# Optimization experiments

Hardware: AMD Instinct MI355X
Metric: run time of the kernel (lower is better)

## Reference

```python
import jax, jax.numpy as jnp
import numpy as np

N_WIRES = 4
DIM = 2 ** N_WIRES  # 16
# ZSIGN[w, b] = +1/-1 eigenvalue of Pauli-Z on wire w for basis state b (qubit 0 = MSB)
_bits = np.array([[(b >> (N_WIRES - 1 - w)) & 1 for b in range(DIM)] for w in range(N_WIRES)])
ZSIGN = jnp.asarray(1.0 - 2.0 * _bits, dtype=jnp.float32)  # [4, 16]
CNOT4 = jnp.asarray(np.array([[1, 0, 0, 0], [0, 1, 0, 0], [0, 0, 0, 1], [0, 0, 1, 0]], dtype=np.float32))


def _apply_1q(state, U2, w):
    # state [..., 16]; apply 2x2 gate U2 on wire w
    batch = state.shape[:-1]
    s = state.reshape(batch + (2,) * N_WIRES)
    s = jnp.moveaxis(s, w - N_WIRES, -1)
    s = s @ U2.astype(s.dtype).T
    s = jnp.moveaxis(s, -1, w - N_WIRES)
    return s.reshape(batch + (DIM,))


def _apply_2q(state, U4, c, t):
    # state [..., 16]; apply 4x4 gate U4 on wires (c=control-axis-first, t)
    batch = state.shape[:-1]
    s = state.reshape(batch + (2,) * N_WIRES)
    s = jnp.moveaxis(s, (c - N_WIRES, t - N_WIRES), (-2, -1))
    sh = s.shape
    s = s.reshape(sh[:-2] + (4,))
    s = s @ U4.astype(s.dtype).T
    s = s.reshape(sh)
    s = jnp.moveaxis(s, (-2, -1), (c - N_WIRES, t - N_WIRES))
    return s.reshape(batch + (DIM,))


def _product_state(qs):
    # kron of per-qubit 2-vectors -> [..., 16]
    s = qs[0]
    for q in qs[1:]:
        o = s[..., :, None] * q[..., None, :]
        s = o.reshape(o.shape[:-2] + (o.shape[-2] * o.shape[-1],))
    return s


def _measure_z(state):
    if jnp.iscomplexobj(state):
        probs = state.real ** 2 + state.imag ** 2
    else:
        probs = state ** 2
    return probs.astype(jnp.float32) @ ZSIGN.T  # [..., 4]


def _quanv(x, rl_params):
    # x [B, 784]; 2x2 stride-2 patches of 28x28 image, RY encode, fixed 8-op
    # 'random layer' (RY(rl_params[w]) on wire w then CNOT(w, w+1 mod 4)), measure Z.
    B = x.shape[0]
    img = x.reshape(B, 14, 2, 14, 2)
    patches = img.transpose(0, 1, 3, 2, 4).reshape(B, 196, 4)  # [(r,c),(r,c+1),(r+1,c),(r+1,c+1)]
    half = patches * 0.5
    q = jnp.stack([jnp.cos(half), jnp.sin(half)], axis=-1)  # RY(theta)|0> is real, [B,196,4,2]
    st = _product_state([q[..., w, :] for w in range(N_WIRES)])  # [B,196,16] float32
    for w in range(N_WIRES):
        th = rl_params[w] * 0.5
        ct, sn = jnp.cos(th), jnp.sin(th)
        U2 = jnp.stack([jnp.stack([ct, -sn]), jnp.stack([sn, ct])])
        st = _apply_1q(st, U2, w)
        st = _apply_2q(st, CNOT4, w, (w + 1) % N_WIRES)
    return _measure_z(st)  # [B, 196, 4]


def _qlayer(ang, theta):
    # RX(ang_w) encode + trainable RX(theta_w) fuse into RX(ang+theta); CNOT ring; <Z>
    half = (ang + theta) * 0.5  # [B, 4]
    c = jnp.cos(half).astype(jnp.complex64)
    s = (-1j) * jnp.sin(half).astype(jnp.complex64)
    q = jnp.stack([c, s], axis=-1)  # [B, 4, 2]
    st = _product_state([q[:, w, :] for w in range(N_WIRES)])  # [B, 16] complex64
    for w in range(N_WIRES):
        st = _apply_2q(st, CNOT4, w, (w + 1) % N_WIRES)
    return _measure_z(st)  # [B, 4]


def _forward(x, rl_params, lin_W, lin_b, qtheta):
    B = x.shape[0]
    qfeat = _quanv(x, rl_params)  # [B, 196, 4]
    xs = jnp.transpose(qfeat, (1, 0, 2))  # [196, B, 4] sequence for quantum LSTM
    h0 = jnp.zeros((B, 4), jnp.float32)
    c0 = jnp.zeros((B, 4), jnp.float32)

    def step(carry, xt):
        hx, cx = carry
        comb = jnp.concatenate([xt, hx], axis=1)  # [B, 8]
        f = jax.nn.sigmoid(_qlayer(comb @ lin_W[0] + lin_b[0], qtheta[0]))
        i = jax.nn.sigmoid(_qlayer(comb @ lin_W[1] + lin_b[1], qtheta[1]))
        g = jnp.tanh(_qlayer(comb @ lin_W[2] + lin_b[2], qtheta[2]))
        o = jax.nn.sigmoid(_qlayer(comb @ lin_W[3] + lin_b[3], qtheta[3]))
        cx = f * cx + i * g
        hx = o * jnp.tanh(cx)
        return (hx, cx), hx

    (hx, cx), _ = jax.lax.scan(step, (h0, c0), xs)
    # torch.tensor([float(v) ...]) detaches -> stop_gradient; mean over batch
    w = jax.lax.stop_gradient(jnp.mean(hx, axis=0))  # [4]
    # EstimatorQNN: ry(inp_i) then rx(w_i) per qubit, observable ZZZZ -> prod cos(inp)cos(w)
    inp = x[:, :N_WIRES]
    return jnp.prod(jnp.cos(inp) * jnp.cos(w), axis=1, keepdims=True)  # [B, 1]


def setup_inputs() -> dict:
    key = jax.random.key(0)
    k0, k1, k2, k3 = jax.random.split(key, 4)
    B = 8192
    x = jax.random.uniform(k0, (B, 784), dtype=jnp.float32) * np.float32(np.pi)
    rl_params = jax.random.normal(k1, (4,), dtype=jnp.float32)
    lin_W = jax.random.normal(k2, (4, 8, 4), dtype=jnp.float32) * np.float32(1.0 / np.sqrt(8.0))
    lin_b = jnp.zeros((4, 4), dtype=jnp.float32)
    qtheta = jax.random.normal(k3, (4, 4), dtype=jnp.float32)
    return {"x": x, "rl_params": rl_params, "lin_W": lin_W, "lin_b": lin_b, "qtheta": qtheta}


def reference(x, rl_params, lin_W, lin_b, qtheta):
    return _forward(x, rl_params, lin_W, lin_b, qtheta)
```

## Files before the change

kernel.cpp:

```cpp
#include <hip/hip_runtime.h>
#include <math.h>

#define NPATCH 196
#define QROWS  204

typedef unsigned short ushort_t;

__device__ __forceinline__ float fast_rcp(float x) { return __builtin_amdgcn_rcpf(x); }

__device__ __forceinline__ ushort_t f2bf(float f) {
    unsigned u = __float_as_uint(f);
    u += 0x7FFFu + ((u >> 16) & 1u);
    return (ushort_t)(u >> 16);
}
__device__ __forceinline__ float bflo(unsigned v) { return __uint_as_float(v << 16); }
__device__ __forceinline__ float bfhi(unsigned v) { return __uint_as_float(v & 0xFFFF0000u); }

template<int CTRL>
__device__ __forceinline__ int dpp_i(int x) {
    return __builtin_amdgcn_update_dpp(x, x, CTRL, 0xF, 0xF, true);
}
template<int CTRL>
__device__ __forceinline__ float dpp_f(float x) {
    return __int_as_float(dpp_i<CTRL>(__float_as_int(x)));
}
#define QP_BCAST0 0x00
#define QP_BCAST1 0x55
#define QP_BCAST2 0xAA
#define QP_BCAST3 0xFF
#define ROR4      0x124
#define ROR8      0x128
#define ROR12     0x12C

#define SPB  16
#define ROWP 788

__global__ __launch_bounds__(256) void quanv_kernel(const float* __restrict__ x,
                                                    const float* __restrict__ rl,
                                                    ushort_t* __restrict__ qfeat, int B)
{
    __shared__ float tile[SPB][ROWP];
    const int tid = threadIdx.x;
    const int b0  = blockIdx.x * SPB;

#pragma unroll 4
    for (int r = 0; r < SPB; ++r) {
        if (tid < 196) {
            ((float4*)&tile[r][0])[tid] =
                ((const float4*)(x + (size_t)(b0 + r) * 784))[tid];
        }
    }
    __syncthreads();

    float rs[4], rc[4];
#pragma unroll
    for (int w = 0; w < 4; ++w) __sincosf(rl[w] * 0.5f, &rs[w], &rc[w]);

    const int s  = tid & 15;
    const int tg = tid >> 4;
    const float* row = &tile[s][0];

    for (int t = tg; t < NPATCH; t += 16) {
        int i = t / 14, j = t - i * 14;
        int o = i * 56 + j * 2;
        float a[4] = { row[o], row[o + 1], row[o + 28], row[o + 29] };

        float cw[4], sw[4];
#pragma unroll
        for (int w = 0; w < 4; ++w) __sincosf(a[w] * 0.5f, &sw[w], &cw[w]);

        float amp[16];
#pragma unroll
        for (int idx = 0; idx < 16; ++idx) {
            float v = ((idx & 8) ? sw[0] : cw[0]) * ((idx & 4) ? sw[1] : cw[1]);
            v *= ((idx & 2) ? sw[2] : cw[2]);
            v *= ((idx & 1) ? sw[3] : cw[3]);
            amp[idx] = v;
        }

#pragma unroll
        for (int w = 0; w < 4; ++w) {
            const int mask = 8 >> w;
#pragma unroll
            for (int idx = 0; idx < 16; ++idx) {
                if (!(idx & mask)) {
                    float a0 = amp[idx], a1 = amp[idx | mask];
                    amp[idx]        = rc[w] * a0 - rs[w] * a1;
                    amp[idx | mask] = rs[w] * a0 + rc[w] * a1;
                }
            }
            const int tmask = 8 >> ((w + 1) & 3);
#pragma unroll
            for (int idx = 0; idx < 16; ++idx) {
                if ((idx & mask) && !(idx & tmask)) {
                    float tmp = amp[idx];
                    amp[idx] = amp[idx | tmask];
                    amp[idx | tmask] = tmp;
                }
            }
        }

        float p[16];
#pragma unroll
        for (int idx = 0; idx < 16; ++idx) p[idx] = amp[idx] * amp[idx];
        float z0 = 0.f, z1 = 0.f, z2 = 0.f, z3 = 0.f;
#pragma unroll
        for (int idx = 0; idx < 16; ++idx) {
            z0 += (idx & 8) ? -p[idx] : p[idx];
            z1 += (idx & 4) ? -p[idx] : p[idx];
            z2 += (idx & 2) ? -p[idx] : p[idx];
            z3 += (idx & 1) ? -p[idx] : p[idx];
        }

        ushort4 outv;
        outv.x = f2bf(z0); outv.y = f2bf(z1); outv.z = f2bf(z2); outv.w = f2bf(z3);
        *(ushort4*)(qfeat + ((size_t)t * B + (b0 + s)) * 4) = outv;
    }
}

__global__ __launch_bounds__(256) void lstm_kernel(const ushort_t* __restrict__ qfeat,
                                                   const float* __restrict__ lin_W,
                                                   const float* __restrict__ lin_b,
                                                   const float* __restrict__ qtheta,
                                                   float* __restrict__ sums, int B)
{
    const int tid = threadIdx.x;
    const int gid = blockIdx.x * 256 + tid;
    const int pr  = gid >> 4;
    const int u   = (tid >> 2) & 3;
    const int k   = tid & 3;
    const int Bh  = B >> 1;

    const int j1 = dpp_i<ROR4>(u);
    const int j2 = dpp_i<ROR8>(u);
    const int j3 = dpp_i<ROR12>(u);

    const float Wx0 = lin_W[(k * 8 + 0) * 4 + u];
    const float Wx1 = lin_W[(k * 8 + 1) * 4 + u];
    const float Wx2 = lin_W[(k * 8 + 2) * 4 + u];
    const float Wx3 = lin_W[(k * 8 + 3) * 4 + u];
    const float Wh0 = lin_W[(k * 8 + 4 + u)  * 4 + u];
    const float Wh1 = lin_W[(k * 8 + 4 + j1) * 4 + u];
    const float Wh2 = lin_W[(k * 8 + 4 + j2) * 4 + u];
    const float Wh3 = lin_W[(k * 8 + 4 + j3) * 4 + u];
    const float bt  = lin_b[k * 4 + u] + qtheta[k * 4 + u];

    auto in_set = [](int j, int uu) {
        return (uu == 0) ? (j != 0) : (uu == 1) ? (j <= 1) : (uu == 2) ? (j <= 2) : true;
    };
    const bool inc0 = in_set(u,  u);
    const bool inc1 = in_set(j1, u);
    const bool inc2 = in_set(j2, u);
    const bool inc3 = in_set(j3, u);

    const float mlt = (k == 2) ?  2.0f : -1.0f;
    const float ga  = (k == 2) ? -2.0f :  1.0f;
    const float gb  = (k == 2) ?  1.0f :  0.0f;

    const uint4* qp = (const uint4*)qfeat;
    uint4 r0 = qp[(size_t)0 * Bh + pr];
    uint4 r1 = qp[(size_t)1 * Bh + pr];
    uint4 r2 = qp[(size_t)2 * Bh + pr];
    uint4 r3 = qp[(size_t)3 * Bh + pr];
    uint4 r4 = qp[(size_t)4 * Bh + pr];
    uint4 r5 = qp[(size_t)5 * Bh + pr];
    uint4 r6 = qp[(size_t)6 * Bh + pr];

    float cxa = 0.f, hxa = 0.f;
    float cxb = 0.f, hxb = 0.f;

    auto step = [&](uint4& buf, int tn) {
        float ax0 = bflo(buf.x), ax1 = bfhi(buf.x), ax2 = bflo(buf.y), ax3 = bfhi(buf.y);
        float bx0 = bflo(buf.z), bx1 = bfhi(buf.z), bx2 = bflo(buf.w), bx3 = bfhi(buf.w);
        buf = qp[(size_t)tn * Bh + pr];

        float ha1 = dpp_f<ROR4>(hxa), hb1 = dpp_f<ROR4>(hxb);
        float ha2 = dpp_f<ROR8>(hxa), hb2 = dpp_f<ROR8>(hxb);
        float ha3 = dpp_f<ROR12>(hxa), hb3 = dpp_f<ROR12>(hxb);

        float as0 = fmaf(ax0, Wx0, bt);
        float bs0 = fmaf(bx0, Wx0, bt);
        float as1 = ax1 * Wx1;
        float bs1 = bx1 * Wx1;
        as0 = fmaf(ax2, Wx2, as0);  bs0 = fmaf(bx2, Wx2, bs0);
        as1 = fmaf(ax3, Wx3, as1);  bs1 = fmaf(bx3, Wx3, bs1);
        as0 = fmaf(hxa, Wh0, as0);  bs0 = fmaf(hxb, Wh0, bs0);
        as1 = fmaf(ha1, Wh1, as1);  bs1 = fmaf(hb1, Wh1, bs1);
        as0 = fmaf(ha2, Wh2, as0);  bs0 = fmaf(hb2, Wh2, bs0);
        as1 = fmaf(ha3, Wh3, as1);  bs1 = fmaf(hb3, Wh3, bs1);
        float cva = __cosf(as0 + as1);
        float cvb = __cosf(bs0 + bs1);

        float ca1 = dpp_f<ROR4>(cva),  cb1 = dpp_f<ROR4>(cvb);
        float ca2 = dpp_f<ROR8>(cva),  cb2 = dpp_f<ROR8>(cvb);
        float ca3 = dpp_f<ROR12>(cva), cb3 = dpp_f<ROR12>(cvb);
        float za = (inc0 ? cva : 1.0f) * (inc1 ? ca1 : 1.0f)
                 * ((inc2 ? ca2 : 1.0f) * (inc3 ? ca3 : 1.0f));
        float zb = (inc0 ? cvb : 1.0f) * (inc1 ? cb1 : 1.0f)
                 * ((inc2 ? cb2 : 1.0f) * (inc3 ? cb3 : 1.0f));

        float ea  = __expf(za * mlt);
        float eb  = __expf(zb * mlt);
        float gva = fmaf(fast_rcp(1.0f + ea), ga, gb);
        float gvb = fmaf(fast_rcp(1.0f + eb), ga, gb);

        float fa = dpp_f<QP_BCAST0>(gva), fb = dpp_f<QP_BCAST0>(gvb);
        float ia = dpp_f<QP_BCAST1>(gva), ib = dpp_f<QP_BCAST1>(gvb);
        float g_a = dpp_f<QP_BCAST2>(gva), g_b = dpp_f<QP_BCAST2>(gvb);
        float oa = dpp_f<QP_BCAST3>(gva), ob = dpp_f<QP_BCAST3>(gvb);

        cxa = fmaf(fa, cxa, ia * g_a);
        cxb = fmaf(fb, cxb, ib * g_b);
        float ta = fmaf(-2.0f, fast_rcp(1.0f + __expf(2.0f * cxa)), 1.0f);
        float tb = fmaf(-2.0f, fast_rcp(1.0f + __expf(2.0f * cxb)), 1.0f);
        hxa = oa * ta;
        hxb = ob * tb;
    };

    for (int t = 0; t < NPATCH; t += 7) {
        step(r0, t + 7);
        step(r1, t + 8);
        step(r2, t + 9);
        step(r3, t + 10);
        step(r4, t + 11);
        step(r5, t + 12);
        step(r6, t + 13);
    }

    float v = hxa + hxb;
    v += __shfl_xor(v, 16, 64);
    v += __shfl_xor(v, 32, 64);
    if ((tid & 63) < 16 && k == 0) atomicAdd(sums + u, v);
}

__global__ __launch_bounds__(256) void final_kernel(const float* __restrict__ x,
                                                    const float* __restrict__ sums,
                                                    float* __restrict__ out,
                                                    int B, float invB)
{
    int b = blockIdx.x * blockDim.x + threadIdx.x;
    if (b >= B) return;
    float P = cosf(sums[0] * invB) * cosf(sums[1] * invB) *
              cosf(sums[2] * invB) * cosf(sums[3] * invB);
    const float4 xi = *(const float4*)(x + (size_t)b * 784);
    out[b] = P * cosf(xi.x) * cosf(xi.y) * cosf(xi.z) * cosf(xi.w);
}

extern "C" void kernel_launch(void* const* d_in, const int* in_sizes, int n_in,
                              void* d_out, int out_size, void* d_ws, size_t ws_size,
                              hipStream_t stream)
{
    const float* x      = (const float*)d_in[0];
    const float* rl     = (const float*)d_in[1];
    const float* lin_W  = (const float*)d_in[2];
    const float* lin_b  = (const float*)d_in[3];
    const float* qtheta = (const float*)d_in[4];
    float* out = (float*)d_out;
    int B = in_sizes[0] / 784;

    float*    sums  = (float*)d_ws;
    ushort_t* qfeat = (ushort_t*)((char*)d_ws + 256);

    hipMemsetAsync(sums, 0, 4 * sizeof(float), stream);

    quanv_kernel<<<B / SPB, 256, 0, stream>>>(x, rl, qfeat, B);

    lstm_kernel<<<(B * 8) / 256, 256, 0, stream>>>(qfeat, lin_W, lin_b, qtheta, sums, B);

    final_kernel<<<(B + 255) / 256, 256, 0, stream>>>(x, sums, out, B, 1.0f / (float)B);
}
```

Baseline: 146.7 us.

## Fuse quanvolution and LSTM kernels through shared-memory feature staging

Merges the quanvolution kernel and the LSTM kernel into one kernel. Each block computes bf16 patch features for 32 samples into shared memory and then runs the recurrent scan from LDS rather than from a global intermediate buffer. This removes the global write and read of the feature tensor and one kernel launch. In exchange the block now reads x directly from global memory with strided float2 loads, and occupancy drops to 256 blocks of 256 threads with a large LDS footprint. The serial LSTM phase can no longer overlap with feature computation of other blocks on the same CU.

```diff
diff --git a/kernel.cpp b/kernel.cpp
--- a/kernel.cpp
+++ b/kernel.cpp
@@ -2,7 +2,7 @@
 #include <math.h>
 
 #define NPATCH 196
-#define QROWS  204
+#define TPAD   202
 
 typedef unsigned short ushort_t;
 
@@ -32,104 +32,95 @@
 #define ROR8      0x128
 #define ROR12     0x12C
 
-#define SPB  16
-#define ROWP 788
-
-__global__ __launch_bounds__(256) void quanv_kernel(const float* __restrict__ x,
-                                                    const float* __restrict__ rl,
-                                                    ushort_t* __restrict__ qfeat, int B)
+__global__ __launch_bounds__(256, 1) void fused_kernel(
+        const float* __restrict__ x,
+        const float* __restrict__ rl,
+        const float* __restrict__ lin_W,
+        const float* __restrict__ lin_b,
+        const float* __restrict__ qtheta,
+        float* __restrict__ sums, int B)
 {
-    __shared__ float tile[SPB][ROWP];
+    __shared__ alignas(16) ushort_t feat[16][TPAD][8];
+
     const int tid = threadIdx.x;
-    const int b0  = blockIdx.x * SPB;
-
-#pragma unroll 4
-    for (int r = 0; r < SPB; ++r) {
-        if (tid < 196) {
-            ((float4*)&tile[r][0])[tid] =
-                ((const float4*)(x + (size_t)(b0 + r) * 784))[tid];
+
+    {
+        const int sb    = tid >> 3;
+        const int tsub  = tid & 7;
+        const int smp   = blockIdx.x * 32 + sb;
+        const int pairb = sb >> 1;
+        const int par   = sb & 1;
+
+        float rs[4], rc[4];
+#pragma unroll
+        for (int w = 0; w < 4; ++w) __sincosf(rl[w] * 0.5f, &rs[w], &rc[w]);
+
+        const float* row = x + (size_t)smp * 784;
+
+        for (int jt = 0; jt < 25; ++jt) {
+            int t = tsub + (jt << 3);
+            if (t < NPATCH) {
+                int i = t / 14, j = t - i * 14;
+                int o = i * 56 + j * 2;
+                float2 p01 = *(const float2*)(row + o);
+                float2 p23 = *(const float2*)(row + o + 28);
+                float a[4] = { p01.x, p01.y, p23.x, p23.y };
+
+                float cw[4], sw[4];
+#pragma unroll
+                for (int w = 0; w < 4; ++w) __sincosf(a[w] * 0.5f, &sw[w], &cw[w]);
+
+                float amp[16];
+#pragma unroll
+                for (int idx = 0; idx < 16; ++idx) {
+                    float v = ((idx & 8) ? sw[0] : cw[0]) * ((idx & 4) ? sw[1] : cw[1]);
+                    v *= ((idx & 2) ? sw[2] : cw[2]);
+                    v *= ((idx & 1) ? sw[3] : cw[3]);
+                    amp[idx] = v;
+                }
+#pragma unroll
+                for (int w = 0; w < 4; ++w) {
+                    const int mask = 8 >> w;
+#pragma unroll
+                    for (int idx = 0; idx < 16; ++idx) {
+                        if (!(idx & mask)) {
+                            float a0 = amp[idx], a1 = amp[idx | mask];
+                            amp[idx]        = rc[w] * a0 - rs[w] * a1;
+                            amp[idx | mask] = rs[w] * a0 + rc[w] * a1;
+                        }
+                    }
+                    const int tmask = 8 >> ((w + 1) & 3);
+#pragma unroll
+                    for (int idx = 0; idx < 16; ++idx) {
+                        if ((idx & mask) && !(idx & tmask)) {
+                            float tmp = amp[idx];
+                            amp[idx] = amp[idx | tmask];
+                            amp[idx | tmask] = tmp;
+                        }
+                    }
+                }
+                float p[16];
+#pragma unroll
+                for (int idx = 0; idx < 16; ++idx) p[idx] = amp[idx] * amp[idx];
+                float z0 = 0.f, z1 = 0.f, z2 = 0.f, z3 = 0.f;
+#pragma unroll
+                for (int idx = 0; idx < 16; ++idx) {
+                    z0 += (idx & 8) ? -p[idx] : p[idx];
+                    z1 += (idx & 4) ? -p[idx] : p[idx];
+                    z2 += (idx & 2) ? -p[idx] : p[idx];
+                    z3 += (idx & 1) ? -p[idx] : p[idx];
+                }
+                ushort4 ov;
+                ov.x = f2bf(z0); ov.y = f2bf(z1); ov.z = f2bf(z2); ov.w = f2bf(z3);
+                *(ushort4*)&feat[pairb][t][par * 4] = ov;
+            }
         }
     }
     __syncthreads();
 
-    float rs[4], rc[4];
-#pragma unroll
-    for (int w = 0; w < 4; ++w) __sincosf(rl[w] * 0.5f, &rs[w], &rc[w]);
-
-    const int s  = tid & 15;
-    const int tg = tid >> 4;
-    const float* row = &tile[s][0];
-
-    for (int t = tg; t < NPATCH; t += 16) {
-        int i = t / 14, j = t - i * 14;
-        int o = i * 56 + j * 2;
-        float a[4] = { row[o], row[o + 1], row[o + 28], row[o + 29] };
-
-        float cw[4], sw[4];
-#pragma unroll
-        for (int w = 0; w < 4; ++w) __sincosf(a[w] * 0.5f, &sw[w], &cw[w]);
-
-        float amp[16];
-#pragma unroll
-        for (int idx = 0; idx < 16; ++idx) {
-            float v = ((idx & 8) ? sw[0] : cw[0]) * ((idx & 4) ? sw[1] : cw[1]);
-            v *= ((idx & 2) ? sw[2] : cw[2]);
-            v *= ((idx & 1) ? sw[3] : cw[3]);
-            amp[idx] = v;
-        }
-
-#pragma unroll
-        for (int w = 0; w < 4; ++w) {
-            const int mask = 8 >> w;
-#pragma unroll
-            for (int idx = 0; idx < 16; ++idx) {
-                if (!(idx & mask)) {
-                    float a0 = amp[idx], a1 = amp[idx | mask];
-                    amp[idx]        = rc[w] * a0 - rs[w] * a1;
-                    amp[idx | mask] = rs[w] * a0 + rc[w] * a1;
-                }
-            }
-            const int tmask = 8 >> ((w + 1) & 3);
-#pragma unroll
-            for (int idx = 0; idx < 16; ++idx) {
-                if ((idx & mask) && !(idx & tmask)) {
-                    float tmp = amp[idx];
-                    amp[idx] = amp[idx | tmask];
-                    amp[idx | tmask] = tmp;
-                }
-            }
-        }
-
-        float p[16];
-#pragma unroll
-        for (int idx = 0; idx < 16; ++idx) p[idx] = amp[idx] * amp[idx];
-        float z0 = 0.f, z1 = 0.f, z2 = 0.f, z3 = 0.f;
-#pragma unroll
-        for (int idx = 0; idx < 16; ++idx) {
-            z0 += (idx & 8) ? -p[idx] : p[idx];
-            z1 += (idx & 4) ? -p[idx] : p[idx];
-            z2 += (idx & 2) ? -p[idx] : p[idx];
-            z3 += (idx & 1) ? -p[idx] : p[idx];
-        }
-
-        ushort4 outv;
-        outv.x = f2bf(z0); outv.y = f2bf(z1); outv.z = f2bf(z2); outv.w = f2bf(z3);
-        *(ushort4*)(qfeat + ((size_t)t * B + (b0 + s)) * 4) = outv;
-    }
-}
-
-__global__ __launch_bounds__(256) void lstm_kernel(const ushort_t* __restrict__ qfeat,
-                                                   const float* __restrict__ lin_W,
-                                                   const float* __restrict__ lin_b,
-                                                   const float* __restrict__ qtheta,
-                                                   float* __restrict__ sums, int B)
-{
-    const int tid = threadIdx.x;
-    const int gid = blockIdx.x * 256 + tid;
-    const int pr  = gid >> 4;
-    const int u   = (tid >> 2) & 3;
-    const int k   = tid & 3;
-    const int Bh  = B >> 1;
+    const int pr = tid >> 4;
+    const int u  = (tid >> 2) & 3;
+    const int k  = tid & 3;
 
     const int j1 = dpp_i<ROR4>(u);
     const int j2 = dpp_i<ROR8>(u);
@@ -157,25 +148,20 @@
     const float ga  = (k == 2) ? -2.0f :  1.0f;
     const float gb  = (k == 2) ?  1.0f :  0.0f;
 
-    const uint4* qp = (const uint4*)qfeat;
-    uint4 r0 = qp[(size_t)0 * Bh + pr];
-    uint4 r1 = qp[(size_t)1 * Bh + pr];
-    uint4 r2 = qp[(size_t)2 * Bh + pr];
-    uint4 r3 = qp[(size_t)3 * Bh + pr];
-    uint4 r4 = qp[(size_t)4 * Bh + pr];
-    uint4 r5 = qp[(size_t)5 * Bh + pr];
-    uint4 r6 = qp[(size_t)6 * Bh + pr];
-
     float cxa = 0.f, hxa = 0.f;
     float cxb = 0.f, hxb = 0.f;
 
-    auto step = [&](uint4& buf, int tn) {
-        float ax0 = bflo(buf.x), ax1 = bfhi(buf.x), ax2 = bflo(buf.y), ax3 = bfhi(buf.y);
-        float bx0 = bflo(buf.z), bx1 = bfhi(buf.z), bx2 = bflo(buf.w), bx3 = bfhi(buf.w);
-        buf = qp[(size_t)tn * Bh + pr];
-
-        float ha1 = dpp_f<ROR4>(hxa), hb1 = dpp_f<ROR4>(hxb);
-        float ha2 = dpp_f<ROR8>(hxa), hb2 = dpp_f<ROR8>(hxb);
+    uint4 cur = *(const uint4*)&feat[pr][0][0];
+
+#pragma unroll 4
+    for (int t = 0; t < NPATCH; ++t) {
+        uint4 nxt = *(const uint4*)&feat[pr][t + 1][0];
+
+        float ax0 = bflo(cur.x), ax1 = bfhi(cur.x), ax2 = bflo(cur.y), ax3 = bfhi(cur.y);
+        float bx0 = bflo(cur.z), bx1 = bfhi(cur.z), bx2 = bflo(cur.w), bx3 = bfhi(cur.w);
+
+        float ha1 = dpp_f<ROR4>(hxa),  hb1 = dpp_f<ROR4>(hxb);
+        float ha2 = dpp_f<ROR8>(hxa),  hb2 = dpp_f<ROR8>(hxb);
         float ha3 = dpp_f<ROR12>(hxa), hb3 = dpp_f<ROR12>(hxb);
 
         float as0 = fmaf(ax0, Wx0, bt);
@@ -194,9 +180,9 @@
         float ca1 = dpp_f<ROR4>(cva),  cb1 = dpp_f<ROR4>(cvb);
         float ca2 = dpp_f<ROR8>(cva),  cb2 = dpp_f<ROR8>(cvb);
         float ca3 = dpp_f<ROR12>(cva), cb3 = dpp_f<ROR12>(cvb);
-        float za = (inc0 ? cva : 1.0f) * (inc1 ? ca1 : 1.0f)
+        float za = ((inc0 ? cva : 1.0f) * (inc1 ? ca1 : 1.0f))
                  * ((inc2 ? ca2 : 1.0f) * (inc3 ? ca3 : 1.0f));
-        float zb = (inc0 ? cvb : 1.0f) * (inc1 ? cb1 : 1.0f)
+        float zb = ((inc0 ? cvb : 1.0f) * (inc1 ? cb1 : 1.0f))
                  * ((inc2 ? cb2 : 1.0f) * (inc3 ? cb3 : 1.0f));
 
         float ea  = __expf(za * mlt);
@@ -215,16 +201,8 @@
         float tb = fmaf(-2.0f, fast_rcp(1.0f + __expf(2.0f * cxb)), 1.0f);
         hxa = oa * ta;
         hxb = ob * tb;
-    };
-
-    for (int t = 0; t < NPATCH; t += 7) {
-        step(r0, t + 7);
-        step(r1, t + 8);
-        step(r2, t + 9);
-        step(r3, t + 10);
-        step(r4, t + 11);
-        step(r5, t + 12);
-        step(r6, t + 13);
+
+        cur = nxt;
     }
 
     float v = hxa + hxb;
@@ -258,14 +236,11 @@
     float* out = (float*)d_out;
     int B = in_sizes[0] / 784;
 
-    float*    sums  = (float*)d_ws;
-    ushort_t* qfeat = (ushort_t*)((char*)d_ws + 256);
+    float* sums = (float*)d_ws;
 
     hipMemsetAsync(sums, 0, 4 * sizeof(float), stream);
 
-    quanv_kernel<<<B / SPB, 256, 0, stream>>>(x, rl, qfeat, B);
-
-    lstm_kernel<<<(B * 8) / 256, 256, 0, stream>>>(qfeat, lin_W, lin_b, qtheta, sums, B);
+    fused_kernel<<<B / 32, 256, 0, stream>>>(x, rl, lin_W, lin_b, qtheta, sums, B);
 
     final_kernel<<<(B + 255) / 256, 256, 0, stream>>>(x, sums, out, B, 1.0f / (float)B);
 }
```

Result: no change. 144.2 us (-1.6%).
